# Kernel tuning notes

Hardware: AMD Instinct MI355X
Metric: run time of the kernel (lower is better)

The kernel has to match this reference:

```python
import jax, jax.numpy as jnp
import numpy as np

B, H, S, D = 2, 16, 2048, 64

def setup_inputs() -> dict:
    key = jax.random.key(0)
    k1, k2, k3 = jax.random.split(key, 3)
    Q = jax.random.normal(k1, (B, H, S, D), dtype=jnp.float32)
    K = jax.random.normal(k2, (B, H, S, D), dtype=jnp.float32)
    V = jax.random.normal(k3, (B, H, S, D), dtype=jnp.float32)
    mask = jnp.zeros((S, S), dtype=bool)  # original default: all-False mask
    return {"Q": Q, "K": K, "V": V, "mask": mask}

def reference(Q, K, V, mask) -> jnp.ndarray:
    # Faithful to the original: dk is the KEY SEQUENCE LENGTH (K.size(-2)),
    # and masked_fill(-1e10) happens BEFORE dividing by sqrt(dk).
    dk = K.shape[-2]
    scores = jnp.einsum('bhqd,bhkd->bhqk', Q, K)          # [B,H,S,S]
    scores = jnp.where(mask, -1e10, scores) / jnp.sqrt(jnp.float32(dk))
    attn = jax.nn.softmax(scores, axis=-1)
    return jnp.einsum('bhqk,bhkd->bhqd', attn, V)
```

## Files before the change

### kernel.cpp

```cpp
#include <hip/hip_runtime.h>

#define SQ   2048
#define DD   64
#define BK   64
#define BQ   128
#define NT   32

typedef _Float16 f16x8 __attribute__((ext_vector_type(8)));
typedef _Float16 f16x4 __attribute__((ext_vector_type(4)));
typedef _Float16 f16x2 __attribute__((ext_vector_type(2)));
typedef float    f32x4 __attribute__((ext_vector_type(4)));

#if __has_builtin(__builtin_amdgcn_exp2f)
#define EXP2F(x) __builtin_amdgcn_exp2f(x)
#else
#define EXP2F(x) exp2f(x)
#endif

static __device__ __forceinline__ f16x2 PKRTZ(float a, float b) {
    typedef __fp16 fp16x2_t __attribute__((ext_vector_type(2)));
    union { fp16x2_t i; f16x2 o; } u;
    u.i = __builtin_amdgcn_cvt_pkrtz(a, b);
    return u.o;
}
#define MFMA32(a, b, c) __builtin_amdgcn_mfma_f32_16x16x32_f16((a), (b), (c), 0, 0, 0)

#define SWZ(row, idx) ((idx) ^ (((row) & 7) << 3))

__global__ __launch_bounds__(256, 2)
void attn_fused9(const float* __restrict__ Qg,
                 const float* __restrict__ Kg,
                 const float* __restrict__ Vg,
                 const unsigned char* __restrict__ maskg,
                 float* __restrict__ Og)
{
    __shared__ _Float16 Kl[2][BK * DD];
    __shared__ _Float16 Vt[2][DD * DD];

    const int tid  = threadIdx.x;
    const int lane = tid & 63;
    const int w    = tid >> 6;
    const int quad = lane >> 4;
    const int l16  = lane & 15;

    const int n     = blockIdx.x;
    const int bh    = (n & 7) + 8 * ((n >> 3) & 3);
    const int qtile = n >> 5;
    const int qBase = qtile * BQ;

    const float QSCALE = 0.02209708691207961f * 1.4426950408889634f;
    const float MASKED = -1e10f * (0.02209708691207961f * 1.4426950408889634f);

    f16x8 qf[2][2];
#pragma unroll
    for (int qg = 0; qg < 2; ++qg) {
        const float* qrow = Qg + ((size_t)bh * SQ + qBase + w * 32 + qg * 16 + l16) * DD;
#pragma unroll
        for (int h = 0; h < 2; ++h) {
            float4 a = *(const float4*)(qrow + h * 32 + quad * 8);
            float4 b = *(const float4*)(qrow + h * 32 + quad * 8 + 4);
            union { f16x8 v; f16x2 p[4]; } u;
            u.p[0] = PKRTZ(a.x * QSCALE, a.y * QSCALE);
            u.p[1] = PKRTZ(a.z * QSCALE, a.w * QSCALE);
            u.p[2] = PKRTZ(b.x * QSCALE, b.y * QSCALE);
            u.p[3] = PKRTZ(b.z * QSCALE, b.w * QSCALE);
            qf[qg][h] = u.v;
        }
    }

    f32x4 acc[2][4];
#pragma unroll
    for (int qg = 0; qg < 2; ++qg)
#pragma unroll
        for (int d = 0; d < 4; ++d) acc[qg][d] = (f32x4){0.f, 0.f, 0.f, 0.f};
    float lsum[2] = {0.f, 0.f};

    const int sr  = tid >> 2;
    const int sc4 = (tid & 3) * 16;
    const int vq  = tid & 15;
    const int vdb = (tid >> 4) * 4;
    const int ctw  = vq >> 2, qdw = vq & 3;
    const int keyp = (ctw >> 1) * 32 + qdw * 8 + (ctw & 1) * 4;

    const float* Kbase = Kg + (size_t)bh * SQ * DD;
    const float* Vbase = Vg + (size_t)bh * SQ * DD;
    const unsigned char* mbase = maskg + (size_t)(qBase + (tid >> 1)) * SQ + (tid & 1) * 32;

    {
        const float* ks = Kbase + (size_t)sr * DD + sc4;
        float4 k0v = *(const float4*)(ks + 0), k1v = *(const float4*)(ks + 4);
        float4 k2v = *(const float4*)(ks + 8), k3v = *(const float4*)(ks + 12);
        float4 v0, v1, v2, v3;
        v0 = *(const float4*)(Vbase + (size_t)(vq * 4 + 0) * DD + vdb);
        v1 = *(const float4*)(Vbase + (size_t)(vq * 4 + 1) * DD + vdb);
        v2 = *(const float4*)(Vbase + (size_t)(vq * 4 + 2) * DD + vdb);
        v3 = *(const float4*)(Vbase + (size_t)(vq * 4 + 3) * DD + vdb);
        union { f16x8 v; f16x2 p[4]; } y0, y1;
        y0.p[0] = PKRTZ(k0v.x, k0v.y); y0.p[1] = PKRTZ(k0v.z, k0v.w);
        y0.p[2] = PKRTZ(k1v.x, k1v.y); y0.p[3] = PKRTZ(k1v.z, k1v.w);
        y1.p[0] = PKRTZ(k2v.x, k2v.y); y1.p[1] = PKRTZ(k2v.z, k2v.w);
        y1.p[2] = PKRTZ(k3v.x, k3v.y); y1.p[3] = PKRTZ(k3v.z, k3v.w);
        *(f16x8*)&Kl[0][SWZ(sr, sr * DD + sc4)]     = y0.v;
        *(f16x8*)&Kl[0][SWZ(sr, sr * DD + sc4 + 8)] = y1.v;
        union { f16x4 v; f16x2 p[2]; } t;
        t.p[0] = PKRTZ(v0.x, v1.x); t.p[1] = PKRTZ(v2.x, v3.x);
        *(f16x4*)&Vt[0][SWZ(vdb + 0, (vdb + 0) * DD + keyp)] = t.v;
        t.p[0] = PKRTZ(v0.y, v1.y); t.p[1] = PKRTZ(v2.y, v3.y);
        *(f16x4*)&Vt[0][SWZ(vdb + 1, (vdb + 1) * DD + keyp)] = t.v;
        t.p[0] = PKRTZ(v0.z, v1.z); t.p[1] = PKRTZ(v2.z, v3.z);
        *(f16x4*)&Vt[0][SWZ(vdb + 2, (vdb + 2) * DD + keyp)] = t.v;
        t.p[0] = PKRTZ(v0.w, v1.w); t.p[1] = PKRTZ(v2.w, v3.w);
        *(f16x4*)&Vt[0][SWZ(vdb + 3, (vdb + 3) * DD + keyp)] = t.v;
    }
    uint4 ma = *(const uint4*)(mbase), mb = *(const uint4*)(mbase + 16);
    int tm = __any((int)(ma.x | ma.y | ma.z | ma.w | mb.x | mb.y | mb.z | mb.w));
    __syncthreads();

#pragma unroll 2
    for (int kt = 0; kt < NT; ++kt) {
        const int cur = kt & 1;
        const bool more = (kt + 1 < NT);

        float4 kx[4], vx[4]; uint4 ma2 = {0,0,0,0}, mb2 = {0,0,0,0};
        if (more) {
            const int k0n = (kt + 1) * BK;
            const float* ks = Kbase + (size_t)(k0n + sr) * DD + sc4;
            kx[0] = *(const float4*)(ks + 0);  kx[1] = *(const float4*)(ks + 4);
            kx[2] = *(const float4*)(ks + 8);  kx[3] = *(const float4*)(ks + 12);
            const float* vb = Vbase + (size_t)(k0n + vq * 4) * DD + vdb;
            vx[0] = *(const float4*)(vb);           vx[1] = *(const float4*)(vb + DD);
            vx[2] = *(const float4*)(vb + 2 * DD);  vx[3] = *(const float4*)(vb + 3 * DD);
            ma2 = *(const uint4*)(mbase + k0n);
            mb2 = *(const uint4*)(mbase + k0n + 16);
        }

        f32x4 sA[4], sB[4];
#pragma unroll
        for (int ct = 0; ct < 4; ++ct) {
            const int krow = ct * 16 + l16;
            f16x8 kf0 = *(const f16x8*)&Kl[cur][SWZ(krow, krow * DD + quad * 8)];
            f16x8 kf1 = *(const f16x8*)&Kl[cur][SWZ(krow, krow * DD + 32 + quad * 8)];
            f32x4 c0 = (f32x4){0.f, 0.f, 0.f, 0.f};
            c0 = MFMA32(kf0, qf[0][0], c0);
            c0 = MFMA32(kf1, qf[0][1], c0);
            sA[ct] = c0;
            f32x4 c1 = (f32x4){0.f, 0.f, 0.f, 0.f};
            c1 = MFMA32(kf0, qf[1][0], c1);
            c1 = MFMA32(kf1, qf[1][1], c1);
            sB[ct] = c1;
        }

        if (tm) {
#pragma unroll
            for (int qg = 0; qg < 2; ++qg) {
                const int qgq = qBase + w * 32 + qg * 16 + l16;
#pragma unroll
                for (int ct = 0; ct < 4; ++ct)
#pragma unroll
                    for (int r = 0; r < 4; ++r) {
                        const int kg = kt * BK + ct * 16 + quad * 4 + r;
                        if (maskg[(size_t)qgq * SQ + kg]) {
                            if (qg == 0) sA[ct][r] = MASKED; else sB[ct][r] = MASKED;
                        }
                    }
            }
        }

        union { f16x8 v; f16x2 p[4]; } pfA[2], pfB[2];
        float ls0 = 0.f, ls1 = 0.f;
#pragma unroll
        for (int ct = 0; ct < 4; ++ct) {
            float a0 = EXP2F(sA[ct][0]), a1 = EXP2F(sA[ct][1]);
            float a2 = EXP2F(sA[ct][2]), a3 = EXP2F(sA[ct][3]);
            float b0 = EXP2F(sB[ct][0]), b1 = EXP2F(sB[ct][1]);
            float b2 = EXP2F(sB[ct][2]), b3 = EXP2F(sB[ct][3]);
            ls0 += (a0 + a1) + (a2 + a3);
            ls1 += (b0 + b1) + (b2 + b3);
            pfA[ct >> 1].p[(ct & 1) * 2 + 0] = PKRTZ(a0, a1);
            pfA[ct >> 1].p[(ct & 1) * 2 + 1] = PKRTZ(a2, a3);
            pfB[ct >> 1].p[(ct & 1) * 2 + 0] = PKRTZ(b0, b1);
            pfB[ct >> 1].p[(ct & 1) * 2 + 1] = PKRTZ(b2, b3);
        }
        lsum[0] += ls0; lsum[1] += ls1;

#pragma unroll
        for (int dt = 0; dt < 4; ++dt) {
#pragma unroll
            for (int cp = 0; cp < 2; ++cp) {
                const int vrow = dt * 16 + l16;
                f16x8 vv = *(const f16x8*)&Vt[cur][SWZ(vrow, vrow * DD + cp * 32 + quad * 8)];
                acc[0][dt] = MFMA32(pfA[cp].v, vv, acc[0][dt]);
                acc[1][dt] = MFMA32(pfB[cp].v, vv, acc[1][dt]);
            }
        }

        if (more) {
            union { f16x8 v; f16x2 p[4]; } y0, y1;
            y0.p[0] = PKRTZ(kx[0].x, kx[0].y); y0.p[1] = PKRTZ(kx[0].z, kx[0].w);
            y0.p[2] = PKRTZ(kx[1].x, kx[1].y); y0.p[3] = PKRTZ(kx[1].z, kx[1].w);
            y1.p[0] = PKRTZ(kx[2].x, kx[2].y); y1.p[1] = PKRTZ(kx[2].z, kx[2].w);
            y1.p[2] = PKRTZ(kx[3].x, kx[3].y); y1.p[3] = PKRTZ(kx[3].z, kx[3].w);
            *(f16x8*)&Kl[cur ^ 1][SWZ(sr, sr * DD + sc4)]     = y0.v;
            *(f16x8*)&Kl[cur ^ 1][SWZ(sr, sr * DD + sc4 + 8)] = y1.v;
            union { f16x4 v; f16x2 p[2]; } t;
            t.p[0] = PKRTZ(vx[0].x, vx[1].x); t.p[1] = PKRTZ(vx[2].x, vx[3].x);
            *(f16x4*)&Vt[cur ^ 1][SWZ(vdb + 0, (vdb + 0) * DD + keyp)] = t.v;
            t.p[0] = PKRTZ(vx[0].y, vx[1].y); t.p[1] = PKRTZ(vx[2].y, vx[3].y);
            *(f16x4*)&Vt[cur ^ 1][SWZ(vdb + 1, (vdb + 1) * DD + keyp)] = t.v;
            t.p[0] = PKRTZ(vx[0].z, vx[1].z); t.p[1] = PKRTZ(vx[2].z, vx[3].z);
            *(f16x4*)&Vt[cur ^ 1][SWZ(vdb + 2, (vdb + 2) * DD + keyp)] = t.v;
            t.p[0] = PKRTZ(vx[0].w, vx[1].w); t.p[1] = PKRTZ(vx[2].w, vx[3].w);
            *(f16x4*)&Vt[cur ^ 1][SWZ(vdb + 3, (vdb + 3) * DD + keyp)] = t.v;
        }
        tm = __any((int)(ma2.x | ma2.y | ma2.z | ma2.w | mb2.x | mb2.y | mb2.z | mb2.w));
        __syncthreads();
    }

#pragma unroll
    for (int qg = 0; qg < 2; ++qg) {
        float l = lsum[qg];
        l += __shfl_xor(l, 16);
        l += __shfl_xor(l, 32);
        float lrow[4];
#pragma unroll
        for (int r = 0; r < 4; ++r) lrow[r] = __shfl(l, quad * 4 + r);
        float* ob = Og + ((size_t)bh * SQ + qBase + w * 32 + qg * 16) * DD;
#pragma unroll
        for (int r = 0; r < 4; ++r) {
            const float inv = 1.0f / lrow[r];
            const int qr = quad * 4 + r;
#pragma unroll
            for (int dt = 0; dt < 4; ++dt)
                ob[qr * DD + dt * 16 + l16] = acc[qg][dt][r] * inv;
        }
    }
}

extern "C" void kernel_launch(void* const* d_in, const int* in_sizes, int n_in,
                              void* d_out, int out_size, void* d_ws, size_t ws_size,
                              hipStream_t stream) {
    const float* Q = (const float*)d_in[0];
    const float* K = (const float*)d_in[1];
    const float* V = (const float*)d_in[2];
    const unsigned char* mask = (const unsigned char*)d_in[3];
    float* Out = (float*)d_out;
    attn_fused9<<<dim3(32 * 16), dim3(256), 0, stream>>>(Q, K, V, mask, Out);
}
```

Measured before the change: 163.0 us.

## Double key tile to 128, use padded LDS rows, precompute mask-tile bitmap

The key tile grows from 64 to 128 rows, so the loop runs 16 iterations with half as many barriers, and each iteration issues twice as many MFMAs. The XOR swizzle is replaced by padded LDS row strides (72 and 136 halfs) to avoid bank conflicts. Mask occupancy per tile is now scanned once up front into a bitmask instead of being prefetched every iteration. Global loads for the next tile are no longer issued before the compute, so load latency is less hidden, and the larger per-iteration live state may add register pressure.

```diff
diff --git a/kernel.cpp b/kernel.cpp
--- a/kernel.cpp
+++ b/kernel.cpp
@@ -2,9 +2,11 @@
 
 #define SQ   2048
 #define DD   64
-#define BK   64
+#define BK   128
 #define BQ   128
-#define NT   32
+#define LDW  72
+#define LDWV 136
+#define NT   16
 
 typedef _Float16 f16x8 __attribute__((ext_vector_type(8)));
 typedef _Float16 f16x4 __attribute__((ext_vector_type(4)));
@@ -25,17 +27,15 @@
 }
 #define MFMA32(a, b, c) __builtin_amdgcn_mfma_f32_16x16x32_f16((a), (b), (c), 0, 0, 0)
 
-#define SWZ(row, idx) ((idx) ^ (((row) & 7) << 3))
-
 __global__ __launch_bounds__(256, 2)
-void attn_fused9(const float* __restrict__ Qg,
+void attn_fusedA(const float* __restrict__ Qg,
                  const float* __restrict__ Kg,
                  const float* __restrict__ Vg,
                  const unsigned char* __restrict__ maskg,
                  float* __restrict__ Og)
 {
-    __shared__ _Float16 Kl[2][BK * DD];
-    __shared__ _Float16 Vt[2][DD * DD];
+    __shared__ _Float16 Kl[2][BK * LDW];
+    __shared__ _Float16 Vt[2][DD * LDWV];
 
     const int tid  = threadIdx.x;
     const int lane = tid & 63;
@@ -75,71 +75,80 @@
         for (int d = 0; d < 4; ++d) acc[qg][d] = (f32x4){0.f, 0.f, 0.f, 0.f};
     float lsum[2] = {0.f, 0.f};
 
-    const int sr  = tid >> 2;
-    const int sc4 = (tid & 3) * 16;
-    const int vq  = tid & 15;
-    const int vdb = (tid >> 4) * 4;
+    const int sr  = tid >> 1;
+    const int sc4 = (tid & 1) * 32;
+    const int vq  = tid & 31;
+    const int vdb = (tid >> 5) * 8;
     const int ctw  = vq >> 2, qdw = vq & 3;
     const int keyp = (ctw >> 1) * 32 + qdw * 8 + (ctw & 1) * 4;
 
     const float* Kbase = Kg + (size_t)bh * SQ * DD;
     const float* Vbase = Vg + (size_t)bh * SQ * DD;
-    const unsigned char* mbase = maskg + (size_t)(qBase + (tid >> 1)) * SQ + (tid & 1) * 32;
-
-    {
-        const float* ks = Kbase + (size_t)sr * DD + sc4;
-        float4 k0v = *(const float4*)(ks + 0), k1v = *(const float4*)(ks + 4);
-        float4 k2v = *(const float4*)(ks + 8), k3v = *(const float4*)(ks + 12);
-        float4 v0, v1, v2, v3;
-        v0 = *(const float4*)(Vbase + (size_t)(vq * 4 + 0) * DD + vdb);
-        v1 = *(const float4*)(Vbase + (size_t)(vq * 4 + 1) * DD + vdb);
-        v2 = *(const float4*)(Vbase + (size_t)(vq * 4 + 2) * DD + vdb);
-        v3 = *(const float4*)(Vbase + (size_t)(vq * 4 + 3) * DD + vdb);
-        union { f16x8 v; f16x2 p[4]; } y0, y1;
-        y0.p[0] = PKRTZ(k0v.x, k0v.y); y0.p[1] = PKRTZ(k0v.z, k0v.w);
-        y0.p[2] = PKRTZ(k1v.x, k1v.y); y0.p[3] = PKRTZ(k1v.z, k1v.w);
-        y1.p[0] = PKRTZ(k2v.x, k2v.y); y1.p[1] = PKRTZ(k2v.z, k2v.w);
-        y1.p[2] = PKRTZ(k3v.x, k3v.y); y1.p[3] = PKRTZ(k3v.z, k3v.w);
-        *(f16x8*)&Kl[0][SWZ(sr, sr * DD + sc4)]     = y0.v;
-        *(f16x8*)&Kl[0][SWZ(sr, sr * DD + sc4 + 8)] = y1.v;
-        union { f16x4 v; f16x2 p[2]; } t;
-        t.p[0] = PKRTZ(v0.x, v1.x); t.p[1] = PKRTZ(v2.x, v3.x);
-        *(f16x4*)&Vt[0][SWZ(vdb + 0, (vdb + 0) * DD + keyp)] = t.v;
-        t.p[0] = PKRTZ(v0.y, v1.y); t.p[1] = PKRTZ(v2.y, v3.y);
-        *(f16x4*)&Vt[0][SWZ(vdb + 1, (vdb + 1) * DD + keyp)] = t.v;
-        t.p[0] = PKRTZ(v0.z, v1.z); t.p[1] = PKRTZ(v2.z, v3.z);
-        *(f16x4*)&Vt[0][SWZ(vdb + 2, (vdb + 2) * DD + keyp)] = t.v;
-        t.p[0] = PKRTZ(v0.w, v1.w); t.p[1] = PKRTZ(v2.w, v3.w);
-        *(f16x4*)&Vt[0][SWZ(vdb + 3, (vdb + 3) * DD + keyp)] = t.v;
-    }
-    uint4 ma = *(const uint4*)(mbase), mb = *(const uint4*)(mbase + 16);
-    int tm = __any((int)(ma.x | ma.y | ma.z | ma.w | mb.x | mb.y | mb.z | mb.w));
+    const unsigned char* mbase = maskg + (size_t)(qBase + (tid >> 1)) * SQ + (tid & 1) * 64;
+
+#define STAGE_K(dstbuf, kofs)                                                      \
+    {                                                                              \
+        const float* ks = Kbase + (size_t)((kofs) + sr) * DD + sc4;                \
+        _Float16* kd = &Kl[dstbuf][sr * LDW + sc4];                                \
+        _Pragma("unroll")                                                          \
+        for (int c = 0; c < 4; ++c) {                                              \
+            float4 x0 = *(const float4*)(ks + c * 8);                              \
+            float4 x1 = *(const float4*)(ks + c * 8 + 4);                          \
+            union { f16x8 v; f16x2 p[4]; } y;                                      \
+            y.p[0] = PKRTZ(x0.x, x0.y); y.p[1] = PKRTZ(x0.z, x0.w);                \
+            y.p[2] = PKRTZ(x1.x, x1.y); y.p[3] = PKRTZ(x1.z, x1.w);                \
+            *(f16x8*)(kd + c * 8) = y.v;                                           \
+        }                                                                          \
+    }
+#define STAGE_V(dstbuf, kofs)                                                      \
+    {                                                                              \
+        const float* vb = Vbase + (size_t)((kofs) + vq * 4) * DD + vdb;            \
+        float4 a0 = *(const float4*)(vb);           float4 a1 = *(const float4*)(vb + 4);            \
+        float4 b0 = *(const float4*)(vb + DD);      float4 b1 = *(const float4*)(vb + DD + 4);       \
+        float4 c0 = *(const float4*)(vb + 2 * DD);  float4 c1 = *(const float4*)(vb + 2 * DD + 4);   \
+        float4 d0 = *(const float4*)(vb + 3 * DD);  float4 d1 = *(const float4*)(vb + 3 * DD + 4);   \
+        union { f16x4 v; f16x2 p[2]; } t;                                          \
+        t.p[0] = PKRTZ(a0.x, b0.x); t.p[1] = PKRTZ(c0.x, d0.x);                    \
+        *(f16x4*)&Vt[dstbuf][(vdb + 0) * LDWV + keyp] = t.v;                       \
+        t.p[0] = PKRTZ(a0.y, b0.y); t.p[1] = PKRTZ(c0.y, d0.y);                    \
+        *(f16x4*)&Vt[dstbuf][(vdb + 1) * LDWV + keyp] = t.v;                       \
+        t.p[0] = PKRTZ(a0.z, b0.z); t.p[1] = PKRTZ(c0.z, d0.z);                    \
+        *(f16x4*)&Vt[dstbuf][(vdb + 2) * LDWV + keyp] = t.v;                       \
+        t.p[0] = PKRTZ(a0.w, b0.w); t.p[1] = PKRTZ(c0.w, d0.w);                    \
+        *(f16x4*)&Vt[dstbuf][(vdb + 3) * LDWV + keyp] = t.v;                       \
+        t.p[0] = PKRTZ(a1.x, b1.x); t.p[1] = PKRTZ(c1.x, d1.x);                    \
+        *(f16x4*)&Vt[dstbuf][(vdb + 4) * LDWV + keyp] = t.v;                       \
+        t.p[0] = PKRTZ(a1.y, b1.y); t.p[1] = PKRTZ(c1.y, d1.y);                    \
+        *(f16x4*)&Vt[dstbuf][(vdb + 5) * LDWV + keyp] = t.v;                       \
+        t.p[0] = PKRTZ(a1.z, b1.z); t.p[1] = PKRTZ(c1.z, d1.z);                    \
+        *(f16x4*)&Vt[dstbuf][(vdb + 6) * LDWV + keyp] = t.v;                       \
+        t.p[0] = PKRTZ(a1.w, b1.w); t.p[1] = PKRTZ(c1.w, d1.w);                    \
+        *(f16x4*)&Vt[dstbuf][(vdb + 7) * LDWV + keyp] = t.v;                       \
+    }
+
+    STAGE_K(0, 0)
+    STAGE_V(0, 0)
+    unsigned tmbits = 0;
+    for (int t = 0; t < NT; ++t) {
+        const unsigned char* mp = mbase + t * BK;
+        uint4 m0 = *(const uint4*)(mp),      m1 = *(const uint4*)(mp + 16);
+        uint4 m2 = *(const uint4*)(mp + 32), m3 = *(const uint4*)(mp + 48);
+        unsigned o = m0.x | m0.y | m0.z | m0.w | m1.x | m1.y | m1.z | m1.w
+                   | m2.x | m2.y | m2.z | m2.w | m3.x | m3.y | m3.z | m3.w;
+        if (__any((int)o)) tmbits |= (1u << t);
+    }
     __syncthreads();
 
-#pragma unroll 2
     for (int kt = 0; kt < NT; ++kt) {
         const int cur = kt & 1;
         const bool more = (kt + 1 < NT);
 
-        float4 kx[4], vx[4]; uint4 ma2 = {0,0,0,0}, mb2 = {0,0,0,0};
-        if (more) {
-            const int k0n = (kt + 1) * BK;
-            const float* ks = Kbase + (size_t)(k0n + sr) * DD + sc4;
-            kx[0] = *(const float4*)(ks + 0);  kx[1] = *(const float4*)(ks + 4);
-            kx[2] = *(const float4*)(ks + 8);  kx[3] = *(const float4*)(ks + 12);
-            const float* vb = Vbase + (size_t)(k0n + vq * 4) * DD + vdb;
-            vx[0] = *(const float4*)(vb);           vx[1] = *(const float4*)(vb + DD);
-            vx[2] = *(const float4*)(vb + 2 * DD);  vx[3] = *(const float4*)(vb + 3 * DD);
-            ma2 = *(const uint4*)(mbase + k0n);
-            mb2 = *(const uint4*)(mbase + k0n + 16);
-        }
-
-        f32x4 sA[4], sB[4];
-#pragma unroll
-        for (int ct = 0; ct < 4; ++ct) {
+        f32x4 sA[8], sB[8];
+#pragma unroll
+        for (int ct = 0; ct < 8; ++ct) {
             const int krow = ct * 16 + l16;
-            f16x8 kf0 = *(const f16x8*)&Kl[cur][SWZ(krow, krow * DD + quad * 8)];
-            f16x8 kf1 = *(const f16x8*)&Kl[cur][SWZ(krow, krow * DD + 32 + quad * 8)];
+            f16x8 kf0 = *(const f16x8*)&Kl[cur][krow * LDW + quad * 8];
+            f16x8 kf1 = *(const f16x8*)&Kl[cur][krow * LDW + 32 + quad * 8];
             f32x4 c0 = (f32x4){0.f, 0.f, 0.f, 0.f};
             c0 = MFMA32(kf0, qf[0][0], c0);
             c0 = MFMA32(kf1, qf[0][1], c0);
@@ -150,12 +159,12 @@
             sB[ct] = c1;
         }
 
-        if (tm) {
+        if ((tmbits >> kt) & 1u) {
 #pragma unroll
             for (int qg = 0; qg < 2; ++qg) {
                 const int qgq = qBase + w * 32 + qg * 16 + l16;
 #pragma unroll
-                for (int ct = 0; ct < 4; ++ct)
+                for (int ct = 0; ct < 8; ++ct)
 #pragma unroll
                     for (int r = 0; r < 4; ++r) {
                         const int kg = kt * BK + ct * 16 + quad * 4 + r;
@@ -166,10 +175,10 @@
             }
         }
 
-        union { f16x8 v; f16x2 p[4]; } pfA[2], pfB[2];
+        union { f16x8 v; f16x2 p[4]; } pfA[4], pfB[4];
         float ls0 = 0.f, ls1 = 0.f;
 #pragma unroll
-        for (int ct = 0; ct < 4; ++ct) {
+        for (int ct = 0; ct < 8; ++ct) {
             float a0 = EXP2F(sA[ct][0]), a1 = EXP2F(sA[ct][1]);
             float a2 = EXP2F(sA[ct][2]), a3 = EXP2F(sA[ct][3]);
             float b0 = EXP2F(sB[ct][0]), b1 = EXP2F(sB[ct][1]);
@@ -185,34 +194,20 @@
 
 #pragma unroll
         for (int dt = 0; dt < 4; ++dt) {
-#pragma unroll
-            for (int cp = 0; cp < 2; ++cp) {
-                const int vrow = dt * 16 + l16;
-                f16x8 vv = *(const f16x8*)&Vt[cur][SWZ(vrow, vrow * DD + cp * 32 + quad * 8)];
+            const int vrow = dt * 16 + l16;
+#pragma unroll
+            for (int cp = 0; cp < 4; ++cp) {
+                f16x8 vv = *(const f16x8*)&Vt[cur][vrow * LDWV + cp * 32 + quad * 8];
                 acc[0][dt] = MFMA32(pfA[cp].v, vv, acc[0][dt]);
                 acc[1][dt] = MFMA32(pfB[cp].v, vv, acc[1][dt]);
             }
         }
 
         if (more) {
-            union { f16x8 v; f16x2 p[4]; } y0, y1;
-            y0.p[0] = PKRTZ(kx[0].x, kx[0].y); y0.p[1] = PKRTZ(kx[0].z, kx[0].w);
-            y0.p[2] = PKRTZ(kx[1].x, kx[1].y); y0.p[3] = PKRTZ(kx[1].z, kx[1].w);
-            y1.p[0] = PKRTZ(kx[2].x, kx[2].y); y1.p[1] = PKRTZ(kx[2].z, kx[2].w);
-            y1.p[2] = PKRTZ(kx[3].x, kx[3].y); y1.p[3] = PKRTZ(kx[3].z, kx[3].w);
-            *(f16x8*)&Kl[cur ^ 1][SWZ(sr, sr * DD + sc4)]     = y0.v;
-            *(f16x8*)&Kl[cur ^ 1][SWZ(sr, sr * DD + sc4 + 8)] = y1.v;
-            union { f16x4 v; f16x2 p[2]; } t;
-            t.p[0] = PKRTZ(vx[0].x, vx[1].x); t.p[1] = PKRTZ(vx[2].x, vx[3].x);
-            *(f16x4*)&Vt[cur ^ 1][SWZ(vdb + 0, (vdb + 0) * DD + keyp)] = t.v;
-            t.p[0] = PKRTZ(vx[0].y, vx[1].y); t.p[1] = PKRTZ(vx[2].y, vx[3].y);
-            *(f16x4*)&Vt[cur ^ 1][SWZ(vdb + 1, (vdb + 1) * DD + keyp)] = t.v;
-            t.p[0] = PKRTZ(vx[0].z, vx[1].z); t.p[1] = PKRTZ(vx[2].z, vx[3].z);
-            *(f16x4*)&Vt[cur ^ 1][SWZ(vdb + 2, (vdb + 2) * DD + keyp)] = t.v;
-            t.p[0] = PKRTZ(vx[0].w, vx[1].w); t.p[1] = PKRTZ(vx[2].w, vx[3].w);
-            *(f16x4*)&Vt[cur ^ 1][SWZ(vdb + 3, (vdb + 3) * DD + keyp)] = t.v;
-        }
-        tm = __any((int)(ma2.x | ma2.y | ma2.z | ma2.w | mb2.x | mb2.y | mb2.z | mb2.w));
+            const int k0n = (kt + 1) * BK;
+            STAGE_K(cur ^ 1, k0n)
+            STAGE_V(cur ^ 1, k0n)
+        }
         __syncthreads();
     }
 
@@ -244,5 +239,5 @@
     const float* V = (const float*)d_in[2];
     const unsigned char* mask = (const unsigned char*)d_in[3];
     float* Out = (float*)d_out;
-    attn_fused9<<<dim3(32 * 16), dim3(256), 0, stream>>>(Q, K, V, mask, Out);
+    attn_fusedA<<<dim3(32 * 16), dim3(256), 0, stream>>>(Q, K, V, mask, Out);
 }
```

Result: no change. 164.1 us (+0.7%).
